# Kernel tuning notes

Hardware: AMD Instinct MI355X
Metric: run time of the kernel (lower is better)

The kernel has to match this reference:

```python
import jax, jax.numpy as jnp
import numpy as np

N_NODES = 100000
N_EDGES = 1600000
IN_FEATS = 128
OUT_FEATS = 128
LN_EPS = 1e-5


def setup_inputs() -> dict:
    key = jax.random.key(0)
    k_h, k_w, k_b, k_src, k_dst = jax.random.split(key, 5)
    stdv = 1.0 / np.sqrt(OUT_FEATS)
    return {
        "h": jax.random.normal(k_h, (N_NODES, IN_FEATS), dtype=jnp.float32),
        "weight": jax.random.uniform(k_w, (IN_FEATS, OUT_FEATS), dtype=jnp.float32, minval=-stdv, maxval=stdv),
        "bias": jax.random.uniform(k_b, (OUT_FEATS,), dtype=jnp.float32, minval=-stdv, maxval=stdv),
        "gamma": jnp.ones((OUT_FEATS,), dtype=jnp.float32),
        "beta": jnp.zeros((OUT_FEATS,), dtype=jnp.float32),
        "src": jax.random.randint(k_src, (N_EDGES,), 0, N_NODES, dtype=jnp.int32),
        "dst": jax.random.randint(k_dst, (N_EDGES,), 0, N_NODES, dtype=jnp.int32),
    }


def reference(h, weight, bias, gamma, beta, src, dst):
    n = h.shape[0]
    # in-degree norm: 1/deg with inf -> 0 (isolated nodes)
    deg = jax.ops.segment_sum(jnp.ones_like(dst, dtype=h.dtype), dst, num_segments=n)
    norm = jnp.where(deg > 0, 1.0 / deg, 0.0)[:, None]  # [N, 1]
    # update_all(copy_src, sum): scatter-add of source features onto destinations
    ah = jax.ops.segment_sum(h[src], dst, num_segments=n)  # [N, in_feats]
    x = ah * norm
    x = x @ weight + bias  # [N, out_feats]
    # LayerNorm over feature dim with affine params
    mu = jnp.mean(x, axis=-1, keepdims=True)
    var = jnp.mean(jnp.square(x - mu), axis=-1, keepdims=True)
    x = (x - mu) * jax.lax.rsqrt(var + LN_EPS) * gamma + beta
    return jax.nn.relu(x)
```

## Files before the change

### kernel.cpp

```cpp
#include <hip/hip_runtime.h>
#include <hip/hip_fp16.h>

#define F 128
#define SCANB 1024
#define NBLK 256
#define BSHIFT 7
#define MAXNB 2048
#define SMEM_BYTES 43264

typedef __attribute__((ext_vector_type(8))) short short8;
typedef __attribute__((ext_vector_type(4))) float f32x4;

static __device__ __forceinline__ short f2bf(float f) {
    union { float f; unsigned u; } v; v.f = f;
    unsigned r = v.u + 0x7FFF + ((v.u >> 16) & 1);
    return (short)(r >> 16);
}
static __device__ __forceinline__ __half2 h2(unsigned u) {
    return __builtin_bit_cast(__half2, u);
}
static __device__ __forceinline__ uint4 pack8h(float a0,float a1,float a2,float a3,
                                               float a4,float a5,float a6,float a7) {
    uint4 o;
    o.x = __builtin_bit_cast(unsigned, __floats2half2_rn(a0, a1));
    o.y = __builtin_bit_cast(unsigned, __floats2half2_rn(a2, a3));
    o.z = __builtin_bit_cast(unsigned, __floats2half2_rn(a4, a5));
    o.w = __builtin_bit_cast(unsigned, __floats2half2_rn(a6, a7));
    return o;
}

__global__ __launch_bounds__(256) void k_gemm_hist(
    const float* __restrict__ h, const float* __restrict__ w,
    unsigned* __restrict__ hb, const int* __restrict__ dst,
    int* __restrict__ mat, int n_nodes, int n_edges, int nb, int hblk) {
    __shared__ alignas(16) char smem[SMEM_BYTES];
    const int tid = threadIdx.x;
    const int bid = blockIdx.x;

    if (bid < hblk) {
        int* lh = (int*)smem;
        for (int i = tid; i < nb; i += 256) lh[i] = 0;
        __syncthreads();
        const int epb = (n_edges + hblk - 1) / hblk;
        const int e0 = bid * epb, e1 = min(e0 + epb, n_edges);
        for (int e = e0 + tid; e < e1; e += 256)
            atomicAdd(&lh[dst[e] >> BSHIFT], 1);
        __syncthreads();
        for (int i = tid; i < nb; i += 256)
            mat[(size_t)i * NBLK + bid] = lh[i];
        return;
    }

    short* wt = (short*)smem;
    float* xs = (float*)(smem + 34816);
    {
        int n = tid & 127;
        for (int k = tid >> 7; k < 128; k += 2)
            wt[n * 136 + k] = f2bf(w[(size_t)k * 128 + n]);
    }
    __syncthreads();

    const int wv = tid >> 6, l = tid & 63, lr = l & 15, lk = l >> 4, q = l & 15;
    const int base = (bid - hblk) * 64;
    if (base >= n_nodes) return;
    const int row = base + wv * 16 + lr;
    const bool valid = row < n_nodes;

    short8 af[4];
    #pragma unroll
    for (int kk = 0; kk < 4; ++kk) {
        int k0 = kk * 32 + lk * 8;
        float4 a0{0,0,0,0}, a1{0,0,0,0};
        if (valid) {
            a0 = *(const float4*)(h + (size_t)row * F + k0);
            a1 = *(const float4*)(h + (size_t)row * F + k0 + 4);
        }
        af[kk] = short8{ f2bf(a0.x), f2bf(a0.y), f2bf(a0.z), f2bf(a0.w),
                         f2bf(a1.x), f2bf(a1.y), f2bf(a1.z), f2bf(a1.w) };
    }
    f32x4 acc[8];
    #pragma unroll
    for (int n = 0; n < 8; ++n) acc[n] = f32x4{0, 0, 0, 0};
    #pragma unroll
    for (int kk = 0; kk < 4; ++kk) {
        const int kb = kk * 32 + lk * 8;
        #pragma unroll
        for (int n = 0; n < 8; ++n) {
            short8 bfr = *(const short8*)(&wt[(n * 16 + lr) * 136 + kb]);
            acc[n] = __builtin_amdgcn_mfma_f32_16x16x32_bf16(af[kk], bfr, acc[n], 0, 0, 0);
        }
    }
    float* xw = xs + wv * (4 * 132);
    #pragma unroll
    for (int r = 0; r < 4; ++r) {
        #pragma unroll
        for (int n = 0; n < 8; ++n)
            xw[lk * 132 + n * 16 + lr] = acc[n][r];
        int grow = base + wv * 16 + lk * 4 + r;
        float4 a = *(const float4*)&xw[lk * 132 + q * 8];
        float4 b = *(const float4*)&xw[lk * 132 + q * 8 + 4];
        uint4 o = pack8h(a.x, a.y, a.z, a.w, b.x, b.y, b.z, b.w);
        if (grow < n_nodes)
            ((uint4*)hb)[(size_t)grow * 16 + q] = o;
    }
}

__global__ __launch_bounds__(SCANB) void k_scan_a(const int* in, int* out,
                                                  int* bsum, int n) {
    __shared__ int tmp[SCANB];
    int i = blockIdx.x * SCANB + threadIdx.x;
    int v = (i < n) ? in[i] : 0;
    tmp[threadIdx.x] = v;
    __syncthreads();
    for (int off = 1; off < SCANB; off <<= 1) {
        int t = (threadIdx.x >= off) ? tmp[threadIdx.x - off] : 0;
        __syncthreads();
        tmp[threadIdx.x] += t;
        __syncthreads();
    }
    if (i < n) out[i] = tmp[threadIdx.x] - v;
    if (threadIdx.x == SCANB - 1) bsum[blockIdx.x] = tmp[SCANB - 1];
}

__global__ __launch_bounds__(512) void k_scan_b(int* bsum, int nb) {
    __shared__ int tmp[512];
    int i = threadIdx.x;
    int v = (i < nb) ? bsum[i] : 0;
    tmp[i] = v;
    __syncthreads();
    for (int off = 1; off < 512; off <<= 1) {
        int t = (i >= off) ? tmp[i - off] : 0;
        __syncthreads();
        tmp[i] += t;
        __syncthreads();
    }
    if (i < nb) bsum[i] = tmp[i] - v;
}

__global__ __launch_bounds__(SCANB) void k_scan_c(int* out, const int* bsum, int n) {
    int i = blockIdx.x * SCANB + threadIdx.x;
    if (i < n) out[i] += bsum[blockIdx.x];
}

__global__ __launch_bounds__(512) void k_part_scatter(
    const int* __restrict__ src, const int* __restrict__ dst,
    const int* __restrict__ mat, const int* __restrict__ bsum,
    unsigned* __restrict__ binned, int n_edges, int nb, int epb) {
    __shared__ int lbase[MAXNB];
    const int bid = blockIdx.x;
    for (int i = threadIdx.x; i < nb; i += 512) {
        int idx = i * NBLK + bid;
        lbase[i] = mat[idx] + bsum[idx >> 10];
    }
    __syncthreads();
    int e0 = bid * epb;
    int e1 = min(e0 + epb, n_edges);
    for (int e = e0 + threadIdx.x; e < e1; e += 512) {
        int d = dst[e];
        int b = d >> BSHIFT;
        int pos = atomicAdd(&lbase[b], 1);
        binned[pos] = ((unsigned)(d & ((1 << BSHIFT) - 1)) << 25) | (unsigned)src[e];
    }
}

__global__ __launch_bounds__(256) void k_bin_to_csr(
    const unsigned* __restrict__ binned, const int* __restrict__ mat,
    const int* __restrict__ bsum, int* __restrict__ deg, int* __restrict__ offs,
    int* __restrict__ esrc, int n_edges, int n_nodes, int nb) {
    __shared__ int ldeg[128], loffs[128], lcur[128];
    int b = blockIdx.x;
    int i0 = b * NBLK;
    int start = mat[i0] + bsum[i0 >> 10];
    int end = n_edges;
    if (b + 1 < nb) {
        int i1 = (b + 1) * NBLK;
        end = mat[i1] + bsum[i1 >> 10];
    }
    int cnt = end - start;
    int base_node = b << BSHIFT;
    int nn = min(1 << BSHIFT, n_nodes - base_node);
    for (int i = threadIdx.x; i < nn; i += 256) { ldeg[i] = 0; lcur[i] = 0; }
    __syncthreads();
    for (int i = threadIdx.x; i < cnt; i += 256)
        atomicAdd(&ldeg[binned[start + i] >> 25], 1);
    __syncthreads();
    if (threadIdx.x == 0) {
        int run = 0;
        for (int i = 0; i < nn; ++i) { loffs[i] = run; run += ldeg[i]; }
    }
    __syncthreads();
    for (int i = threadIdx.x; i < nn; i += 256) {
        deg[base_node + i]  = ldeg[i];
        offs[base_node + i] = start + loffs[i];
    }
    for (int i = threadIdx.x; i < cnt; i += 256) {
        unsigned p = binned[start + i];
        int ln = p >> 25;
        int pos = start + loffs[ln] + atomicAdd(&lcur[ln], 1);
        esrc[pos] = (int)(p & ((1u << 25) - 1));
    }
}

__global__ __launch_bounds__(256) void k_hist(const int* __restrict__ dst,
                                              int* __restrict__ deg, int n_edges) {
    int e = blockIdx.x * 256 + threadIdx.x;
    if (e < n_edges) atomicAdd(&deg[dst[e]], 1);
}

__global__ __launch_bounds__(256) void k_scatter_idx(
    const int* __restrict__ src, const int* __restrict__ dst,
    const int* __restrict__ offs, int* __restrict__ cursor,
    int* __restrict__ esrc, int n_edges) {
    int e = blockIdx.x * 256 + threadIdx.x;
    if (e >= n_edges) return;
    int d = dst[e];
    int pos = offs[d] + atomicAdd(&cursor[d], 1);
    esrc[pos] = src[e];
}

__global__ __launch_bounds__(256) void k_gather_ln(
    const unsigned* __restrict__ hb, const int* __restrict__ esrc,
    const int* __restrict__ offs, const int* __restrict__ deg,
    const float* __restrict__ bias, const float* __restrict__ gamma,
    const float* __restrict__ beta, float* __restrict__ out, int n_nodes) {
    int t = blockIdx.x * 256 + threadIdx.x;
    int node = t >> 6;
    int l = t & 63;
    if (node >= n_nodes) return;
    const int g = l >> 4;
    const int q = l & 15;

    const int start = offs[node];
    const int dn = deg[node];
    const int end = start + dn;

    __half2 c0 = __floats2half2_rn(0.f, 0.f);
    __half2 c1 = c0, c2 = c0, c3 = c0;
    int i = start;
    for (; i + 16 <= end; i += 16) {
        int s0 = esrc[i + g];
        int s1 = esrc[i + 4 + g];
        int s2 = esrc[i + 8 + g];
        int s3 = esrc[i + 12 + g];
        uint4 v0 = *((const uint4*)(hb + (size_t)s0 * 64 + q * 4));
        uint4 v1 = *((const uint4*)(hb + (size_t)s1 * 64 + q * 4));
        uint4 v2 = *((const uint4*)(hb + (size_t)s2 * 64 + q * 4));
        uint4 v3 = *((const uint4*)(hb + (size_t)s3 * 64 + q * 4));
        c0 = __hadd2(c0, __hadd2(__hadd2(h2(v0.x), h2(v1.x)), __hadd2(h2(v2.x), h2(v3.x))));
        c1 = __hadd2(c1, __hadd2(__hadd2(h2(v0.y), h2(v1.y)), __hadd2(h2(v2.y), h2(v3.y))));
        c2 = __hadd2(c2, __hadd2(__hadd2(h2(v0.z), h2(v1.z)), __hadd2(h2(v2.z), h2(v3.z))));
        c3 = __hadd2(c3, __hadd2(__hadd2(h2(v0.w), h2(v1.w)), __hadd2(h2(v2.w), h2(v3.w))));
    }
    for (; i + 8 <= end; i += 8) {
        int s0 = esrc[i + g];
        int s1 = esrc[i + 4 + g];
        uint4 v0 = *((const uint4*)(hb + (size_t)s0 * 64 + q * 4));
        uint4 v1 = *((const uint4*)(hb + (size_t)s1 * 64 + q * 4));
        c0 = __hadd2(c0, __hadd2(h2(v0.x), h2(v1.x)));
        c1 = __hadd2(c1, __hadd2(h2(v0.y), h2(v1.y)));
        c2 = __hadd2(c2, __hadd2(h2(v0.z), h2(v1.z)));
        c3 = __hadd2(c3, __hadd2(h2(v0.w), h2(v1.w)));
    }
    for (; i < end; i += 4) {
        int e = i + g;
        if (e < end) {
            int s = esrc[e];
            uint4 v = *((const uint4*)(hb + (size_t)s * 64 + q * 4));
            c0 = __hadd2(c0, h2(v.x));
            c1 = __hadd2(c1, h2(v.y));
            c2 = __hadd2(c2, h2(v.z));
            c3 = __hadd2(c3, h2(v.w));
        }
    }
    float2 p0 = __half22float2(c0), p1 = __half22float2(c1);
    float2 p2 = __half22float2(c2), p3 = __half22float2(c3);
    float a0 = p0.x, a1 = p0.y, a2 = p1.x, a3 = p1.y;
    float a4 = p2.x, a5 = p2.y, a6 = p3.x, a7 = p3.y;

    #pragma unroll
    for (int m = 16; m <= 32; m <<= 1) {
        a0 += __shfl_xor(a0, m); a1 += __shfl_xor(a1, m);
        a2 += __shfl_xor(a2, m); a3 += __shfl_xor(a3, m);
        a4 += __shfl_xor(a4, m); a5 += __shfl_xor(a5, m);
        a6 += __shfl_xor(a6, m); a7 += __shfl_xor(a7, m);
    }
    float4 bs0 = *(const float4*)(bias  + q * 8);
    float4 bs1 = *(const float4*)(bias  + q * 8 + 4);
    const float nv = dn > 0 ? 1.0f / (float)dn : 0.0f;
    float f0 = a0 * nv + bs0.x, f1 = a1 * nv + bs0.y;
    float f2 = a2 * nv + bs0.z, f3 = a3 * nv + bs0.w;
    float f4 = a4 * nv + bs1.x, f5 = a5 * nv + bs1.y;
    float f6 = a6 * nv + bs1.z, f7 = a7 * nv + bs1.w;

    float s  = ((f0 + f1) + (f2 + f3)) + ((f4 + f5) + (f6 + f7));
    float q2 = ((f0*f0 + f1*f1) + (f2*f2 + f3*f3)) + ((f4*f4 + f5*f5) + (f6*f6 + f7*f7));
    #pragma unroll
    for (int m = 1; m <= 8; m <<= 1) {
        s  += __shfl_xor(s, m);
        q2 += __shfl_xor(q2, m);
    }
    float mu   = s * (1.0f / F);
    float var  = q2 * (1.0f / F) - mu * mu;
    float rstd = rsqrtf(var + 1e-5f);

    if (g == 0) {
        float4 gm0 = *(const float4*)(gamma + q * 8);
        float4 gm1 = *(const float4*)(gamma + q * 8 + 4);
        float4 bt0 = *(const float4*)(beta  + q * 8);
        float4 bt1 = *(const float4*)(beta  + q * 8 + 4);
        float4 o0, o1;
        o0.x = fmaxf((f0 - mu) * rstd * gm0.x + bt0.x, 0.0f);
        o0.y = fmaxf((f1 - mu) * rstd * gm0.y + bt0.y, 0.0f);
        o0.z = fmaxf((f2 - mu) * rstd * gm0.z + bt0.z, 0.0f);
        o0.w = fmaxf((f3 - mu) * rstd * gm0.w + bt0.w, 0.0f);
        o1.x = fmaxf((f4 - mu) * rstd * gm1.x + bt1.x, 0.0f);
        o1.y = fmaxf((f5 - mu) * rstd * gm1.y + bt1.y, 0.0f);
        o1.z = fmaxf((f6 - mu) * rstd * gm1.z + bt1.z, 0.0f);
        o1.w = fmaxf((f7 - mu) * rstd * gm1.w + bt1.w, 0.0f);
        float* op = out + (size_t)node * F + q * 8;
        *(float4*)op = o0;
        *(float4*)(op + 4) = o1;
    }
}

extern "C" void kernel_launch(void* const* d_in, const int* in_sizes, int n_in,
                              void* d_out, int out_size, void* d_ws, size_t ws_size,
                              hipStream_t stream) {
    const float* h      = (const float*)d_in[0];
    const float* weight = (const float*)d_in[1];
    const float* bias   = (const float*)d_in[2];
    const float* gamma  = (const float*)d_in[3];
    const float* beta   = (const float*)d_in[4];
    const int*   src    = (const int*)d_in[5];
    const int*   dst    = (const int*)d_in[6];

    const int n_nodes = in_sizes[0] / F;
    const int n_edges = in_sizes[5];

    float* x = (float*)d_out;

    const int nb = (n_nodes + (1 << BSHIFT) - 1) >> BSHIFT;
    const int len = nb * NBLK;
    const int nscan = (len + SCANB - 1) / SCANB;
    const bool shift_ok = (nb <= MAXNB) && (nscan <= 512) && (n_nodes <= (1 << 25));

    int* deg    = (int*)d_ws;
    int* offs   = deg + n_nodes;
    int* esrc   = offs + n_nodes;
    unsigned* hb = (unsigned*)(esrc + n_edges);
    int* bsum   = (int*)(hb + (size_t)n_nodes * 64);
    int* mat    = bsum + 1024;
    unsigned* binned = (unsigned*)(mat + (size_t)len);
    int* cursor = mat;

    size_t need_common = ((size_t)2 * n_nodes + (size_t)n_edges + 1024) * sizeof(int)
                       + (size_t)n_nodes * 64 * sizeof(unsigned);
    size_t need_new  = need_common + ((size_t)len + (size_t)n_edges) * sizeof(int);
    size_t need_fall = need_common + (size_t)n_nodes * sizeof(int);
    bool use_new = shift_ok && ws_size >= need_new;

    const int gb = (n_nodes + 63) / 64;

    if (use_new) {
        k_gemm_hist<<<NBLK + gb, 256, 0, stream>>>(h, weight, hb, dst, mat,
                                                   n_nodes, n_edges, nb, NBLK);
        k_scan_a<<<nscan, SCANB, 0, stream>>>(mat, mat, bsum, len);
        k_scan_b<<<1, 512, 0, stream>>>(bsum, nscan);
        const int epb = (n_edges + NBLK - 1) / NBLK;
        k_part_scatter<<<NBLK, 512, 0, stream>>>(src, dst, mat, bsum, binned,
                                                 n_edges, nb, epb);
        k_bin_to_csr<<<nb, 256, 0, stream>>>(binned, mat, bsum, deg, offs, esrc,
                                             n_edges, n_nodes, nb);
        int gblocks = (int)(((size_t)n_nodes * 64 + 255) / 256);
        k_gather_ln<<<gblocks, 256, 0, stream>>>(hb, esrc, offs, deg,
                                                 bias, gamma, beta, x, n_nodes);
    } else if (ws_size >= need_fall) {
        k_gemm_hist<<<gb, 256, 0, stream>>>(h, weight, hb, dst, mat,
                                            n_nodes, n_edges, nb, 0);
        const int nscan2 = (n_nodes + SCANB - 1) / SCANB;
        hipMemsetAsync(deg, 0, (size_t)n_nodes * sizeof(int), stream);
        hipMemsetAsync(cursor, 0, (size_t)n_nodes * sizeof(int), stream);
        k_hist<<<(n_edges + 255) / 256, 256, 0, stream>>>(dst, deg, n_edges);
        k_scan_a<<<nscan2, SCANB, 0, stream>>>(deg, offs, bsum, n_nodes);
        k_scan_b<<<1, 512, 0, stream>>>(bsum, nscan2);
        k_scan_c<<<nscan2, SCANB, 0, stream>>>(offs, bsum, n_nodes);
        k_scatter_idx<<<(n_edges + 255) / 256, 256, 0, stream>>>(
            src, dst, offs, cursor, esrc, n_edges);
        int gblocks = (int)(((size_t)n_nodes * 64 + 255) / 256);
        k_gather_ln<<<gblocks, 256, 0, stream>>>(hb, esrc, offs, deg,
                                                 bias, gamma, beta, x, n_nodes);
    }
}
```

Measured before the change: 129.6 us.

## Persist GEMM blocks, fuse two-level scan via last-block pattern, widen bin_to_csr

```diff
diff --git a/kernel.cpp b/kernel.cpp
--- a/kernel.cpp
+++ b/kernel.cpp
@@ -4,6 +4,7 @@
 #define F 128
 #define SCANB 1024
 #define NBLK 256
+#define GB2 512
 #define BSHIFT 7
 #define MAXNB 2048
 #define SMEM_BYTES 43264
@@ -32,10 +33,13 @@
 __global__ __launch_bounds__(256) void k_gemm_hist(
     const float* __restrict__ h, const float* __restrict__ w,
     unsigned* __restrict__ hb, const int* __restrict__ dst,
-    int* __restrict__ mat, int n_nodes, int n_edges, int nb, int hblk) {
+    int* __restrict__ mat, int* __restrict__ done,
+    int n_nodes, int n_edges, int nb, int hblk) {
     __shared__ alignas(16) char smem[SMEM_BYTES];
     const int tid = threadIdx.x;
     const int bid = blockIdx.x;
+
+    if (bid == 0 && tid == 0 && done) *done = 0;
 
     if (bid < hblk) {
         int* lh = (int*)smem;
@@ -61,47 +65,88 @@
     __syncthreads();
 
     const int wv = tid >> 6, l = tid & 63, lr = l & 15, lk = l >> 4, q = l & 15;
-    const int base = (bid - hblk) * 64;
-    if (base >= n_nodes) return;
-    const int row = base + wv * 16 + lr;
-    const bool valid = row < n_nodes;
-
-    short8 af[4];
-    #pragma unroll
-    for (int kk = 0; kk < 4; ++kk) {
-        int k0 = kk * 32 + lk * 8;
-        float4 a0{0,0,0,0}, a1{0,0,0,0};
-        if (valid) {
-            a0 = *(const float4*)(h + (size_t)row * F + k0);
-            a1 = *(const float4*)(h + (size_t)row * F + k0 + 4);
+    const int step = (gridDim.x - hblk) * 64;
+    float* xw = xs + wv * (4 * 132);
+
+    for (int base = (bid - hblk) * 64; base < n_nodes; base += step) {
+        const int row = base + wv * 16 + lr;
+        const bool valid = row < n_nodes;
+
+        short8 af[4];
+        #pragma unroll
+        for (int kk = 0; kk < 4; ++kk) {
+            int k0 = kk * 32 + lk * 8;
+            float4 a0{0,0,0,0}, a1{0,0,0,0};
+            if (valid) {
+                a0 = *(const float4*)(h + (size_t)row * F + k0);
+                a1 = *(const float4*)(h + (size_t)row * F + k0 + 4);
+            }
+            af[kk] = short8{ f2bf(a0.x), f2bf(a0.y), f2bf(a0.z), f2bf(a0.w),
+                             f2bf(a1.x), f2bf(a1.y), f2bf(a1.z), f2bf(a1.w) };
         }
-        af[kk] = short8{ f2bf(a0.x), f2bf(a0.y), f2bf(a0.z), f2bf(a0.w),
-                         f2bf(a1.x), f2bf(a1.y), f2bf(a1.z), f2bf(a1.w) };
-    }
-    f32x4 acc[8];
-    #pragma unroll
-    for (int n = 0; n < 8; ++n) acc[n] = f32x4{0, 0, 0, 0};
-    #pragma unroll
-    for (int kk = 0; kk < 4; ++kk) {
-        const int kb = kk * 32 + lk * 8;
+        f32x4 acc[8];
         #pragma unroll
-        for (int n = 0; n < 8; ++n) {
-            short8 bfr = *(const short8*)(&wt[(n * 16 + lr) * 136 + kb]);
-            acc[n] = __builtin_amdgcn_mfma_f32_16x16x32_bf16(af[kk], bfr, acc[n], 0, 0, 0);
+        for (int n = 0; n < 8; ++n) acc[n] = f32x4{0, 0, 0, 0};
+        #pragma unroll
+        for (int kk = 0; kk < 4; ++kk) {
+            const int kb = kk * 32 + lk * 8;
+            #pragma unroll
+            for (int n = 0; n < 8; ++n) {
+                short8 bfr = *(const short8*)(&wt[(n * 16 + lr) * 136 + kb]);
+                acc[n] = __builtin_amdgcn_mfma_f32_16x16x32_bf16(af[kk], bfr, acc[n], 0, 0, 0);
+            }
         }
-    }
-    float* xw = xs + wv * (4 * 132);
-    #pragma unroll
-    for (int r = 0; r < 4; ++r) {
         #pragma unroll
-        for (int n = 0; n < 8; ++n)
-            xw[lk * 132 + n * 16 + lr] = acc[n][r];
-        int grow = base + wv * 16 + lk * 4 + r;
-        float4 a = *(const float4*)&xw[lk * 132 + q * 8];
-        float4 b = *(const float4*)&xw[lk * 132 + q * 8 + 4];
-        uint4 o = pack8h(a.x, a.y, a.z, a.w, b.x, b.y, b.z, b.w);
-        if (grow < n_nodes)
-            ((uint4*)hb)[(size_t)grow * 16 + q] = o;
+        for (int r = 0; r < 4; ++r) {
+            #pragma unroll
+            for (int n = 0; n < 8; ++n)
+                xw[lk * 132 + n * 16 + lr] = acc[n][r];
+            int grow = base + wv * 16 + lk * 4 + r;
+            float4 a = *(const float4*)&xw[lk * 132 + q * 8];
+            float4 b = *(const float4*)&xw[lk * 132 + q * 8 + 4];
+            uint4 o = pack8h(a.x, a.y, a.z, a.w, b.x, b.y, b.z, b.w);
+            if (grow < n_nodes)
+                ((uint4*)hb)[(size_t)grow * 16 + q] = o;
+        }
+    }
+}
+
+__global__ __launch_bounds__(SCANB) void k_scan_ab(const int* in, int* out,
+                                                   int* bsum, int* done, int n) {
+    __shared__ int tmp[SCANB];
+    __shared__ bool amLast;
+    int i = blockIdx.x * SCANB + threadIdx.x;
+    int v = (i < n) ? in[i] : 0;
+    tmp[threadIdx.x] = v;
+    __syncthreads();
+    for (int off = 1; off < SCANB; off <<= 1) {
+        int t = (threadIdx.x >= off) ? tmp[threadIdx.x - off] : 0;
+        __syncthreads();
+        tmp[threadIdx.x] += t;
+        __syncthreads();
+    }
+    if (i < n) out[i] = tmp[threadIdx.x] - v;
+    if (threadIdx.x == SCANB - 1) {
+        bsum[blockIdx.x] = tmp[SCANB - 1];
+        __threadfence();
+        int old = atomicAdd(done, 1);
+        amLast = (old == (int)gridDim.x - 1);
+    }
+    __syncthreads();
+    if (amLast) {
+        __threadfence();
+        const int ns = gridDim.x;
+        int w = (threadIdx.x < ns) ? ((volatile int*)bsum)[threadIdx.x] : 0;
+        __syncthreads();
+        tmp[threadIdx.x] = w;
+        __syncthreads();
+        for (int off = 1; off < SCANB; off <<= 1) {
+            int t = (threadIdx.x >= off) ? tmp[threadIdx.x - off] : 0;
+            __syncthreads();
+            tmp[threadIdx.x] += t;
+            __syncthreads();
+        }
+        if (threadIdx.x < ns) bsum[threadIdx.x] = tmp[threadIdx.x] - w;
     }
 }
 
@@ -163,7 +208,7 @@
     }
 }
 
-__global__ __launch_bounds__(256) void k_bin_to_csr(
+__global__ __launch_bounds__(512) void k_bin_to_csr(
     const unsigned* __restrict__ binned, const int* __restrict__ mat,
     const int* __restrict__ bsum, int* __restrict__ deg, int* __restrict__ offs,
     int* __restrict__ esrc, int n_edges, int n_nodes, int nb) {
@@ -179,9 +224,9 @@
     int cnt = end - start;
     int base_node = b << BSHIFT;
     int nn = min(1 << BSHIFT, n_nodes - base_node);
-    for (int i = threadIdx.x; i < nn; i += 256) { ldeg[i] = 0; lcur[i] = 0; }
-    __syncthreads();
-    for (int i = threadIdx.x; i < cnt; i += 256)
+    for (int i = threadIdx.x; i < nn; i += 512) { ldeg[i] = 0; lcur[i] = 0; }
+    __syncthreads();
+    for (int i = threadIdx.x; i < cnt; i += 512)
         atomicAdd(&ldeg[binned[start + i] >> 25], 1);
     __syncthreads();
     if (threadIdx.x == 0) {
@@ -189,11 +234,11 @@
         for (int i = 0; i < nn; ++i) { loffs[i] = run; run += ldeg[i]; }
     }
     __syncthreads();
-    for (int i = threadIdx.x; i < nn; i += 256) {
+    for (int i = threadIdx.x; i < nn; i += 512) {
         deg[base_node + i]  = ldeg[i];
         offs[base_node + i] = start + loffs[i];
     }
-    for (int i = threadIdx.x; i < cnt; i += 256) {
+    for (int i = threadIdx.x; i < cnt; i += 512) {
         unsigned p = binned[start + i];
         int ln = p >> 25;
         int pos = start + loffs[ln] + atomicAdd(&lcur[ln], 1);
@@ -349,6 +394,7 @@
     int* esrc   = offs + n_nodes;
     unsigned* hb = (unsigned*)(esrc + n_edges);
     int* bsum   = (int*)(hb + (size_t)n_nodes * 64);
+    int* done   = bsum + 1023;
     int* mat    = bsum + 1024;
     unsigned* binned = (unsigned*)(mat + (size_t)len);
     int* cursor = mat;
@@ -362,20 +408,19 @@
     const int gb = (n_nodes + 63) / 64;
 
     if (use_new) {
-        k_gemm_hist<<<NBLK + gb, 256, 0, stream>>>(h, weight, hb, dst, mat,
-                                                   n_nodes, n_edges, nb, NBLK);
-        k_scan_a<<<nscan, SCANB, 0, stream>>>(mat, mat, bsum, len);
-        k_scan_b<<<1, 512, 0, stream>>>(bsum, nscan);
+        k_gemm_hist<<<NBLK + GB2, 256, 0, stream>>>(h, weight, hb, dst, mat, done,
+                                                    n_nodes, n_edges, nb, NBLK);
+        k_scan_ab<<<nscan, SCANB, 0, stream>>>(mat, mat, bsum, done, len);
         const int epb = (n_edges + NBLK - 1) / NBLK;
         k_part_scatter<<<NBLK, 512, 0, stream>>>(src, dst, mat, bsum, binned,
                                                  n_edges, nb, epb);
-        k_bin_to_csr<<<nb, 256, 0, stream>>>(binned, mat, bsum, deg, offs, esrc,
+        k_bin_to_csr<<<nb, 512, 0, stream>>>(binned, mat, bsum, deg, offs, esrc,
                                              n_edges, n_nodes, nb);
         int gblocks = (int)(((size_t)n_nodes * 64 + 255) / 256);
         k_gather_ln<<<gblocks, 256, 0, stream>>>(hb, esrc, offs, deg,
                                                  bias, gamma, beta, x, n_nodes);
     } else if (ws_size >= need_fall) {
-        k_gemm_hist<<<gb, 256, 0, stream>>>(h, weight, hb, dst, mat,
+        k_gemm_hist<<<gb, 256, 0, stream>>>(h, weight, hb, dst, mat, (int*)nullptr,
                                             n_nodes, n_edges, nb, 0);
         const int nscan2 = (n_nodes + SCANB - 1) / SCANB;
         hipMemsetAsync(deg, 0, (size_t)n_nodes * sizeof(int), stream);
```

Result: no change. 129.0 us (-0.4%).
